# Optimization experiments

Hardware: AMD Instinct MI355X
Metric: run time of the kernel (lower is better)

The kernel has to match this reference:

```python
import jax, jax.numpy as jnp
import numpy as np

N_FEATURES = 100
D_TOKEN = 192
D_HID = D_TOKEN // 2


def setup_inputs() -> dict:
    key = jax.random.key(0)
    k_x, k_w1, k_b1, k_w2, k_b2 = jax.random.split(key, 5)
    # Per-feature stacked weights (equivalent to n_features separate tiny MLPs).
    # Linear(1, h): weight [h, 1] -> stacked as W1 [F, h]; bias b1 [F, h]
    # Linear(h, d): weight [d, h] -> stacked as W2 [F, h, d]; bias b2 [F, d]
    lim1 = 1.0  # kaiming-uniform bound for fan_in=1: sqrt(1/1)
    lim2 = 1.0 / np.sqrt(D_HID)
    x = jax.random.normal(k_x, (4096, N_FEATURES), dtype=jnp.float32)
    W1 = jax.random.uniform(k_w1, (N_FEATURES, D_HID), jnp.float32, -lim1, lim1)
    b1 = jax.random.uniform(k_b1, (N_FEATURES, D_HID), jnp.float32, -lim1, lim1)
    W2 = jax.random.uniform(k_w2, (N_FEATURES, D_HID, D_TOKEN), jnp.float32, -lim2, lim2)
    b2 = jax.random.uniform(k_b2, (N_FEATURES, D_TOKEN), jnp.float32, -lim2, lim2)
    return {"x": x, "W1": W1, "b1": b1, "W2": W2, "b2": b2}


def reference(x, W1, b1, W2, b2):
    # x: [B, F] scalar per feature
    # hidden: [B, F, H] = x[b,f] * W1[f,h] + b1[f,h]
    h = jax.nn.gelu(x[:, :, None] * W1[None, :, :] + b1[None, :, :], approximate=False)
    # out: [B, F, D] = einsum over hidden dim, one small GEMM per feature batched
    out = jnp.einsum('bfh,fhd->bfd', h, W2) + b2[None, :, :]
    return out
```

## Files before the change

kernel.cpp:

```cpp
#include <hip/hip_runtime.h>
#include <hip/hip_bf16.h>

#define N_F 100
#define N_B 4096
#define DH 96
#define DT 192
#define BM 64
#define HPAD 100

typedef unsigned short u16;
typedef unsigned int u32;
typedef __bf16 bf16x8 __attribute__((ext_vector_type(8)));
typedef float f32x4 __attribute__((ext_vector_type(4)));

union FragAB { bf16x8 v; uint2 q2[2]; uint4 q4; };

static __device__ __forceinline__ u16 f2bf(float v) {
    u32 b = __float_as_uint(v);
    return (u16)((b + 0x7FFFu + ((b >> 16) & 1u)) >> 16);
}

static __device__ __forceinline__ float gelu_fast(float p) {
    float p3 = p * p * p;
    float y  = fmaf(0.044715f, p3, p);
    float t  = exp2f(2.3022083f * y);
    float r  = __builtin_amdgcn_rcpf(1.0f + t);
    return fmaf(-p, r, p);
}

__global__ void convert_w2_kernel(const float* __restrict__ W2, u16* __restrict__ W2F) {
    int idx = blockIdx.x * 256 + threadIdx.x;
    if (idx >= N_F * DH * (DT / 4)) return;
    int f  = idx / (DH * (DT / 4));
    int r  = idx - f * (DH * (DT / 4));
    int k  = r / (DT / 4);
    int d4 = (r - k * (DT / 4)) * 4;
    const float4 w = *(const float4*)&W2[(f * DH + k) * DT + d4];

    int ks = k >> 5;
    int kr = k & 31;
    int q  = (kr >> 2) & 3;
    int e  = ((kr >> 4) << 2) | (kr & 3);
    u16* base = W2F + (size_t)f * (DH * DT);
    int DT16 = d4 >> 4;
    int m    = d4 & 15;
    size_t i0 = ((size_t)(ks * 12 + DT16) * 64 + q * 16 + m) * 8 + e;
    base[i0]      = f2bf(w.x);
    base[i0 + 8]  = f2bf(w.y);
    base[i0 + 16] = f2bf(w.z);
    base[i0 + 24] = f2bf(w.w);
}

template <bool USE_WS>
__global__ __launch_bounds__(256) void mlp_tok_kernel(
    const float* __restrict__ x, const float* __restrict__ W1,
    const float* __restrict__ b1, const float* __restrict__ W2,
    const float* __restrict__ b2, const u16* __restrict__ W2F,
    float* __restrict__ out)
{
    const int f   = blockIdx.x;
    const int b0  = blockIdx.y * BM;
    const int tid = threadIdx.x;
    const int lane = tid & 63;
    const int wv   = tid >> 6;

    __shared__ float x_lds[BM];
    __shared__ u16 h_lds[BM][HPAD];
    __shared__ u16 w2t_lds[USE_WS ? 1 : DT][HPAD];

    if (tid < BM) x_lds[tid] = x[(size_t)(b0 + tid) * N_F + f];
    __syncthreads();

    {
        const int row = tid & (BM - 1);
        const int kc  = (tid >> 6) * 24;
        const float xv = x_lds[row];
        #pragma unroll
        for (int c = 0; c < 6; ++c) {
            const int k = kc + c * 4;
            const float4 w1v = *(const float4*)&W1[f * DH + k];
            const float4 b1v = *(const float4*)&b1[f * DH + k];
            float g0 = gelu_fast(fmaf(xv, w1v.x, b1v.x));
            float g1 = gelu_fast(fmaf(xv, w1v.y, b1v.y));
            float g2 = gelu_fast(fmaf(xv, w1v.z, b1v.z));
            float g3 = gelu_fast(fmaf(xv, w1v.w, b1v.w));
            uint2 pk;
            pk.x = (u32)f2bf(g0) | ((u32)f2bf(g1) << 16);
            pk.y = (u32)f2bf(g2) | ((u32)f2bf(g3) << 16);
            *(uint2*)&h_lds[row][k] = pk;
        }
    }

    if constexpr (!USE_WS) {
        #pragma unroll
        for (int i = 0; i < (DT * DH) / (256 * 4); ++i) {
            const int e = (i * 256 + tid) * 4;
            const int k = e / DT;
            const int n = e - k * DT;
            const float4 wv4 = *(const float4*)&W2[(f * DH + k) * DT + n];
            w2t_lds[n + 0][k] = f2bf(wv4.x);
            w2t_lds[n + 1][k] = f2bf(wv4.y);
            w2t_lds[n + 2][k] = f2bf(wv4.z);
            w2t_lds[n + 3][k] = f2bf(wv4.w);
        }
    }
    __syncthreads();

    const int q = lane >> 4;
    const int m = lane & 15;

    f32x4 acc[3][4];
    #pragma unroll
    for (int dt = 0; dt < 3; ++dt)
        #pragma unroll
        for (int bt = 0; bt < 4; ++bt)
            acc[dt][bt] = (f32x4){0.f, 0.f, 0.f, 0.f};

    const u16* __restrict__ w2ff = USE_WS ? (W2F + (size_t)f * (DH * DT)) : nullptr;

    #pragma unroll
    for (int ks = 0; ks < 3; ++ks) {
        const int k0 = ks * 32 + q * 4;
        FragAB a[3], hb[4];
        #pragma unroll
        for (int dt = 0; dt < 3; ++dt) {
            if constexpr (USE_WS) {
                a[dt].q4 = *(const uint4*)&w2ff[((ks * 12 + wv * 3 + dt) * 64 + lane) * 8];
            } else {
                const int d = wv * 48 + dt * 16 + m;
                a[dt].q2[0] = *(const uint2*)&w2t_lds[d][k0];
                a[dt].q2[1] = *(const uint2*)&w2t_lds[d][k0 + 16];
            }
        }
        #pragma unroll
        for (int bt = 0; bt < 4; ++bt) {
            hb[bt].q2[0] = *(const uint2*)&h_lds[bt * 16 + m][k0];
            hb[bt].q2[1] = *(const uint2*)&h_lds[bt * 16 + m][k0 + 16];
        }
        #pragma unroll
        for (int dt = 0; dt < 3; ++dt)
            #pragma unroll
            for (int bt = 0; bt < 4; ++bt)
                acc[dt][bt] = __builtin_amdgcn_mfma_f32_16x16x32_bf16(
                    a[dt].v, hb[bt].v, acc[dt][bt], 0, 0, 0);
    }

    const int dbase = wv * 48;
    f32x4 b2q[3];
    #pragma unroll
    for (int dt = 0; dt < 3; ++dt)
        b2q[dt] = *(const f32x4*)&b2[f * DT + dbase + dt * 16 + q * 4];

    #pragma unroll
    for (int bt = 0; bt < 4; ++bt) {
        const size_t rowb = ((size_t)(b0 + bt * 16 + m) * N_F + f) * DT + dbase + q * 4;
        #pragma unroll
        for (int dt = 0; dt < 3; ++dt) {
            f32x4 v = acc[dt][bt] + b2q[dt];
            *(f32x4*)&out[rowb + dt * 16] = v;
        }
    }
}

extern "C" void kernel_launch(void* const* d_in, const int* in_sizes, int n_in,
                              void* d_out, int out_size, void* d_ws, size_t ws_size,
                              hipStream_t stream) {
    const float* x  = (const float*)d_in[0];
    const float* W1 = (const float*)d_in[1];
    const float* b1 = (const float*)d_in[2];
    const float* W2 = (const float*)d_in[3];
    const float* b2 = (const float*)d_in[4];
    float* out = (float*)d_out;

    const size_t w2f_bytes = (size_t)N_F * DT * DH * sizeof(u16);
    dim3 grid(N_F, N_B / BM);

    if (ws_size >= w2f_bytes) {
        u16* W2F = (u16*)d_ws;
        convert_w2_kernel<<<(N_F * DH * (DT / 4) + 255) / 256, 256, 0, stream>>>(W2, W2F);
        mlp_tok_kernel<true><<<grid, 256, 0, stream>>>(x, W1, b1, W2, b2, W2F, out);
    } else {
        mlp_tok_kernel<false><<<grid, 256, 0, stream>>>(x, W1, b1, W2, b2, nullptr, out);
    }
}
```

Baseline: 91.01 us.

## Use single-wave blocks of 16 batch rows with register-resident hidden tiles

Each block becomes one 64-lane wave handling 16 batch rows and all 192 output columns, instead of four waves over 64 rows. The GELU hidden tile is computed directly into MFMA B-fragment registers, which removes the h LDS buffer and its barriers. Output goes through an LDS staging buffer so global stores are contiguous rows. The trade-off is four times as many blocks, each re-reading the full per-feature W2 fragment from global memory, which costs much more W2 traffic and less reuse per load.

```diff
diff --git a/kernel.cpp b/kernel.cpp
--- a/kernel.cpp
+++ b/kernel.cpp
@@ -5,8 +5,8 @@
 #define N_B 4096
 #define DH 96
 #define DT 192
-#define BM 64
-#define HPAD 100
+#define BW 16
+#define SPAD 100
 
 typedef unsigned short u16;
 typedef unsigned int u32;
@@ -52,34 +52,30 @@
 }
 
 template <bool USE_WS>
-__global__ __launch_bounds__(256) void mlp_tok_kernel(
+__global__ __launch_bounds__(64, 3) void mlp_tok_kernel(
     const float* __restrict__ x, const float* __restrict__ W1,
     const float* __restrict__ b1, const float* __restrict__ W2,
     const float* __restrict__ b2, const u16* __restrict__ W2F,
     float* __restrict__ out)
 {
-    const int f   = blockIdx.x;
-    const int b0  = blockIdx.y * BM;
-    const int tid = threadIdx.x;
-    const int lane = tid & 63;
-    const int wv   = tid >> 6;
+    const int f    = blockIdx.x;
+    const int b0   = blockIdx.y * BW;
+    const int lane = threadIdx.x;
+    const int q    = lane >> 4;
+    const int m    = lane & 15;
 
-    __shared__ float x_lds[BM];
-    __shared__ u16 h_lds[BM][HPAD];
-    __shared__ u16 w2t_lds[USE_WS ? 1 : DT][HPAD];
+    __shared__ float stage[2][BW][SPAD];
 
-    if (tid < BM) x_lds[tid] = x[(size_t)(b0 + tid) * N_F + f];
-    __syncthreads();
+    const float xv = x[(size_t)(b0 + m) * N_F + f];
 
-    {
-        const int row = tid & (BM - 1);
-        const int kc  = (tid >> 6) * 24;
-        const float xv = x_lds[row];
+    FragAB hb[3];
+    #pragma unroll
+    for (int ks = 0; ks < 3; ++ks) {
         #pragma unroll
-        for (int c = 0; c < 6; ++c) {
-            const int k = kc + c * 4;
-            const float4 w1v = *(const float4*)&W1[f * DH + k];
-            const float4 b1v = *(const float4*)&b1[f * DH + k];
+        for (int hh = 0; hh < 2; ++hh) {
+            const int k0 = ks * 32 + hh * 16 + q * 4;
+            const float4 w1v = *(const float4*)&W1[f * DH + k0];
+            const float4 b1v = *(const float4*)&b1[f * DH + k0];
             float g0 = gelu_fast(fmaf(xv, w1v.x, b1v.x));
             float g1 = gelu_fast(fmaf(xv, w1v.y, b1v.y));
             float g2 = gelu_fast(fmaf(xv, w1v.z, b1v.z));
@@ -87,77 +83,60 @@
             uint2 pk;
             pk.x = (u32)f2bf(g0) | ((u32)f2bf(g1) << 16);
             pk.y = (u32)f2bf(g2) | ((u32)f2bf(g3) << 16);
-            *(uint2*)&h_lds[row][k] = pk;
+            hb[ks].q2[hh] = pk;
         }
     }
 
-    if constexpr (!USE_WS) {
-        #pragma unroll
-        for (int i = 0; i < (DT * DH) / (256 * 4); ++i) {
-            const int e = (i * 256 + tid) * 4;
-            const int k = e / DT;
-            const int n = e - k * DT;
-            const float4 wv4 = *(const float4*)&W2[(f * DH + k) * DT + n];
-            w2t_lds[n + 0][k] = f2bf(wv4.x);
-            w2t_lds[n + 1][k] = f2bf(wv4.y);
-            w2t_lds[n + 2][k] = f2bf(wv4.z);
-            w2t_lds[n + 3][k] = f2bf(wv4.w);
-        }
-    }
-    __syncthreads();
-
-    const int q = lane >> 4;
-    const int m = lane & 15;
-
-    f32x4 acc[3][4];
+    f32x4 acc[12];
     #pragma unroll
-    for (int dt = 0; dt < 3; ++dt)
-        #pragma unroll
-        for (int bt = 0; bt < 4; ++bt)
-            acc[dt][bt] = (f32x4){0.f, 0.f, 0.f, 0.f};
+    for (int dt = 0; dt < 12; ++dt) acc[dt] = (f32x4){0.f, 0.f, 0.f, 0.f};
 
     const u16* __restrict__ w2ff = USE_WS ? (W2F + (size_t)f * (DH * DT)) : nullptr;
 
     #pragma unroll
     for (int ks = 0; ks < 3; ++ks) {
-        const int k0 = ks * 32 + q * 4;
-        FragAB a[3], hb[4];
+        FragAB a[12];
         #pragma unroll
-        for (int dt = 0; dt < 3; ++dt) {
+        for (int dt = 0; dt < 12; ++dt) {
             if constexpr (USE_WS) {
-                a[dt].q4 = *(const uint4*)&w2ff[((ks * 12 + wv * 3 + dt) * 64 + lane) * 8];
+                a[dt].q4 = *(const uint4*)&w2ff[((size_t)(ks * 12 + dt) * 64 + lane) * 8];
             } else {
-                const int d = wv * 48 + dt * 16 + m;
-                a[dt].q2[0] = *(const uint2*)&w2t_lds[d][k0];
-                a[dt].q2[1] = *(const uint2*)&w2t_lds[d][k0 + 16];
+                const int d = dt * 16 + m;
+                u16 tmp[8];
+                #pragma unroll
+                for (int e = 0; e < 8; ++e) {
+                    const int k = ks * 32 + (e >> 2) * 16 + q * 4 + (e & 3);
+                    tmp[e] = f2bf(W2[((size_t)f * DH + k) * DT + d]);
+                }
+                a[dt].q4 = make_uint4(
+                    (u32)tmp[0] | ((u32)tmp[1] << 16), (u32)tmp[2] | ((u32)tmp[3] << 16),
+                    (u32)tmp[4] | ((u32)tmp[5] << 16), (u32)tmp[6] | ((u32)tmp[7] << 16));
             }
         }
         #pragma unroll
-        for (int bt = 0; bt < 4; ++bt) {
-            hb[bt].q2[0] = *(const uint2*)&h_lds[bt * 16 + m][k0];
-            hb[bt].q2[1] = *(const uint2*)&h_lds[bt * 16 + m][k0 + 16];
-        }
-        #pragma unroll
-        for (int dt = 0; dt < 3; ++dt)
-            #pragma unroll
-            for (int bt = 0; bt < 4; ++bt)
-                acc[dt][bt] = __builtin_amdgcn_mfma_f32_16x16x32_bf16(
-                    a[dt].v, hb[bt].v, acc[dt][bt], 0, 0, 0);
+        for (int dt = 0; dt < 12; ++dt)
+            acc[dt] = __builtin_amdgcn_mfma_f32_16x16x32_bf16(
+                a[dt].v, hb[ks].v, acc[dt], 0, 0, 0);
     }
 
-    const int dbase = wv * 48;
-    f32x4 b2q[3];
     #pragma unroll
-    for (int dt = 0; dt < 3; ++dt)
-        b2q[dt] = *(const f32x4*)&b2[f * DT + dbase + dt * 16 + q * 4];
-
-    #pragma unroll
-    for (int bt = 0; bt < 4; ++bt) {
-        const size_t rowb = ((size_t)(b0 + bt * 16 + m) * N_F + f) * DT + dbase + q * 4;
+    for (int h = 0; h < 2; ++h) {
         #pragma unroll
-        for (int dt = 0; dt < 3; ++dt) {
-            f32x4 v = acc[dt][bt] + b2q[dt];
-            *(f32x4*)&out[rowb + dt * 16] = v;
+        for (int dtl = 0; dtl < 6; ++dtl) {
+            const int dt = h * 6 + dtl;
+            const f32x4 bq = *(const f32x4*)&b2[f * DT + dt * 16 + q * 4];
+            f32x4 v = acc[dt] + bq;
+            *(f32x4*)&stage[h][m][dtl * 16 + q * 4] = v;
+        }
+        asm volatile("s_waitcnt lgkmcnt(0)" ::: "memory");
+        __builtin_amdgcn_sched_barrier(0);
+        #pragma unroll
+        for (int i = 0; i < 6; ++i) {
+            const int idx = i * 64 + lane;
+            const int row = idx / 24;
+            const int c4  = idx - row * 24;
+            f32x4 v = *(const f32x4*)&stage[h][row][c4 * 4];
+            *(f32x4*)&out[((size_t)(b0 + row) * N_F + f) * DT + h * 96 + c4 * 4] = v;
         }
     }
 }
@@ -173,13 +152,13 @@
     float* out = (float*)d_out;
 
     const size_t w2f_bytes = (size_t)N_F * DT * DH * sizeof(u16);
-    dim3 grid(N_F, N_B / BM);
+    dim3 grid(N_F, N_B / BW);
 
     if (ws_size >= w2f_bytes) {
         u16* W2F = (u16*)d_ws;
         convert_w2_kernel<<<(N_F * DH * (DT / 4) + 255) / 256, 256, 0, stream>>>(W2, W2F);
-        mlp_tok_kernel<true><<<grid, 256, 0, stream>>>(x, W1, b1, W2, b2, W2F, out);
+        mlp_tok_kernel<true><<<grid, 64, 0, stream>>>(x, W1, b1, W2, b2, W2F, out);
     } else {
-        mlp_tok_kernel<false><<<grid, 256, 0, stream>>>(x, W1, b1, W2, b2, nullptr, out);
+        mlp_tok_kernel<false><<<grid, 64, 0, stream>>>(x, W1, b1, W2, b2, nullptr, out);
     }
 }
```

Result: slower. 93.52 us (+2.8%).
